# Kernel optimization log

Measured on AMD Instinct MI355X. Metric: run time of the kernel, lower is better.

Reference implementation:

```python
import jax, jax.numpy as jnp
import numpy as np

B, S, U = 64, 64, 16
EMB = 10
D = U - 2 + 2 * EMB      # encoder d_model = 34
DD = 3                   # decoder d_model
FF = 4                   # dim_feedforward
NL = 4                   # num layers (enc and dec)
ENH = 2                  # encoder heads
WV, SV = 10000, 400      # word / syllable vocab sizes


def _ln(x, w, b, eps=1e-5):
    mu = jnp.mean(x, -1, keepdims=True)
    var = jnp.mean((x - mu) ** 2, -1, keepdims=True)
    return (x - mu) / jnp.sqrt(var + eps) * w + b


def _mha(xq, xkv, qkv_w, qkv_b, out_w, out_b, nhead, mask=None):
    d = xq.shape[-1]
    wq, wk, wv = jnp.split(qkv_w, 3, axis=0)
    bq, bk, bv = jnp.split(qkv_b, 3, axis=0)
    q = xq @ wq.T + bq
    k = xkv @ wk.T + bk
    v = xkv @ wv.T + bv
    b_, sq, sk = q.shape[0], q.shape[1], k.shape[1]
    dh = d // nhead
    q = q.reshape(b_, sq, nhead, dh)
    k = k.reshape(b_, sk, nhead, dh)
    v = v.reshape(b_, sk, nhead, dh)
    scores = jnp.einsum('bqhd,bkhd->bhqk', q, k) * (1.0 / np.sqrt(dh))
    if mask is not None:
        scores = scores + mask
    attn = jax.nn.softmax(scores, axis=-1)
    out = jnp.einsum('bhqk,bkhd->bqhd', attn, v).reshape(b_, sq, d)
    return out @ out_w.T + out_b


def _pos_encoding(batch, d_model):
    # Faithful to the original quirk: pe has shape [max_len, 1, d] and is added
    # to a batch-first [B,S,D] tensor as x + pe[:B]  ->  row b of pe is added
    # to ALL sequence positions of batch element b.
    pos = jnp.arange(batch, dtype=jnp.float32)[:, None]
    div = jnp.exp(jnp.arange(0, d_model, 2, dtype=jnp.float32) * (-np.log(10000.0) / d_model))
    ang = pos * div  # [B, D/2]
    pe = jnp.stack([jnp.sin(ang), jnp.cos(ang)], axis=-1).reshape(batch, d_model)
    return pe[:, None, :]  # [B,1,D]


def setup_inputs() -> dict:
    key = jax.random.key(0)
    ks = iter(jax.random.split(key, 64))

    def n(shape, s=0.1):
        return jax.random.normal(next(ks), shape, dtype=jnp.float32) * s

    base = jax.random.uniform(next(ks), (B, S, U), dtype=jnp.float32)
    widx = jax.random.randint(next(ks), (B, S), 0, WV).astype(jnp.float32)
    sidx = jax.random.randint(next(ks), (B, S), 0, SV).astype(jnp.float32)
    src = base.at[:, :, U - 2].set(widx).at[:, :, U - 1].set(sidx)
    return {
        'src': src,
        'word_emb': jax.random.uniform(next(ks), (WV, EMB), jnp.float32, -0.1, 0.1),
        'syll_emb': jax.random.uniform(next(ks), (SV, EMB), jnp.float32, -0.1, 0.1),
        'enc_qkv_w': n((NL, 3 * D, D)), 'enc_qkv_b': jnp.zeros((NL, 3 * D)),
        'enc_out_w': n((NL, D, D)), 'enc_out_b': jnp.zeros((NL, D)),
        'enc_ln1_w': jnp.ones((NL, D)), 'enc_ln1_b': jnp.zeros((NL, D)),
        'enc_lin1_w': n((NL, FF, D)), 'enc_lin1_b': jnp.zeros((NL, FF)),
        'enc_lin2_w': n((NL, D, FF)), 'enc_lin2_b': jnp.zeros((NL, D)),
        'enc_ln2_w': jnp.ones((NL, D)), 'enc_ln2_b': jnp.zeros((NL, D)),
        'norm_w': jnp.ones((D,)), 'norm_b': jnp.zeros((D,)),
        'eo_w': jax.random.uniform(next(ks), (DD, D), jnp.float32, -0.1, 0.1),
        'eo_b': jnp.zeros((DD,)),
        'dec_sa_qkv_w': n((NL, 3 * DD, DD)), 'dec_sa_qkv_b': jnp.zeros((NL, 3 * DD)),
        'dec_sa_out_w': n((NL, DD, DD)), 'dec_sa_out_b': jnp.zeros((NL, DD)),
        'dec_ln1_w': jnp.ones((NL, DD)), 'dec_ln1_b': jnp.zeros((NL, DD)),
        'dec_ca_qkv_w': n((NL, 3 * DD, DD)), 'dec_ca_qkv_b': jnp.zeros((NL, 3 * DD)),
        'dec_ca_out_w': n((NL, DD, DD)), 'dec_ca_out_b': jnp.zeros((NL, DD)),
        'dec_ln2_w': jnp.ones((NL, DD)), 'dec_ln2_b': jnp.zeros((NL, DD)),
        'dec_lin1_w': n((NL, FF, DD)), 'dec_lin1_b': jnp.zeros((NL, FF)),
        'dec_lin2_w': n((NL, DD, FF)), 'dec_lin2_b': jnp.zeros((NL, DD)),
        'dec_ln3_w': jnp.ones((NL, DD)), 'dec_ln3_b': jnp.zeros((NL, DD)),
    }


def reference(src, word_emb, syll_emb,
              enc_qkv_w, enc_qkv_b, enc_out_w, enc_out_b,
              enc_ln1_w, enc_ln1_b, enc_lin1_w, enc_lin1_b,
              enc_lin2_w, enc_lin2_b, enc_ln2_w, enc_ln2_b,
              norm_w, norm_b, eo_w, eo_b,
              dec_sa_qkv_w, dec_sa_qkv_b, dec_sa_out_w, dec_sa_out_b,
              dec_ln1_w, dec_ln1_b,
              dec_ca_qkv_w, dec_ca_qkv_b, dec_ca_out_w, dec_ca_out_b,
              dec_ln2_w, dec_ln2_b,
              dec_lin1_w, dec_lin1_b, dec_lin2_w, dec_lin2_b,
              dec_ln3_w, dec_ln3_b):
    b, s = src.shape[0], src.shape[1]
    # embed_lyrics
    widx = src[:, :, U - 2].astype(jnp.int32)
    sidx = src[:, :, U - 1].astype(jnp.int32)
    x = jnp.concatenate([src[:, :, :U - 2], word_emb[widx], syll_emb[sidx]], axis=2)  # [B,S,D]
    x = x + _pos_encoding(b, D)
    # TransformerEncoder (post-norm, relu, dropout=0) + final LayerNorm
    for l in range(NL):
        sa = _mha(x, x, enc_qkv_w[l], enc_qkv_b[l], enc_out_w[l], enc_out_b[l], ENH)
        x = _ln(x + sa, enc_ln1_w[l], enc_ln1_b[l])
        ff = jax.nn.relu(x @ enc_lin1_w[l].T + enc_lin1_b[l]) @ enc_lin2_w[l].T + enc_lin2_b[l]
        x = _ln(x + ff, enc_ln2_w[l], enc_ln2_b[l])
    x = _ln(x, norm_w, norm_b)
    memory = x @ eo_w.T + eo_b  # [B,S,3]

    causal = jnp.where(jnp.tril(jnp.ones((s, s), bool)), 0.0, -1e9).astype(jnp.float32)

    def decode(tgt):
        y = tgt
        for l in range(NL):
            sa = _mha(y, y, dec_sa_qkv_w[l], dec_sa_qkv_b[l], dec_sa_out_w[l], dec_sa_out_b[l], 1, causal)
            y = _ln(y + sa, dec_ln1_w[l], dec_ln1_b[l])
            ca = _mha(y, memory, dec_ca_qkv_w[l], dec_ca_qkv_b[l], dec_ca_out_w[l], dec_ca_out_b[l], 1)
            y = _ln(y + ca, dec_ln2_w[l], dec_ln2_b[l])
            ff = jax.nn.relu(y @ dec_lin1_w[l].T + dec_lin1_b[l]) @ dec_lin2_w[l].T + dec_lin2_b[l]
            y = _ln(y + ff, dec_ln3_w[l], dec_ln3_b[l])
        return y

    # mask, position i only depends on tgt[:, :i+1], so a fixed-size padded
    # buffer + scan computes identical values.
    def step(tgt, i):
        out_i = jax.lax.dynamic_slice_in_dim(decode(tgt), i, 1, axis=1)  # [B,1,3]
        return jax.lax.dynamic_update_slice(tgt, out_i, (0, i + 1, 0)), None

    tgt0 = jnp.zeros((b, s, DD), jnp.float32)
    tgt, _ = jax.lax.scan(step, tgt0, jnp.arange(s - 1))
    return jnp.concatenate([tgt, src[:, :, U - 2:U - 1], src[:, :, U - 1:U]], axis=2)
```

## Files before the change

kernel.cpp:

```cpp
#include <hip/hip_runtime.h>
#include <math.h>

#define B_ 64
#define S_ 64
#define U_ 16
#define EMB_ 10
#define D_ 34
#define DD_ 3
#define FF_ 4
#define NL_ 4

__global__ __launch_bounds__(512) void enc_kernel(
    const float* __restrict__ src, const float* __restrict__ wemb,
    const float* __restrict__ semb,
    const float* __restrict__ qkv_w, const float* __restrict__ qkv_b,
    const float* __restrict__ out_w, const float* __restrict__ out_b,
    const float* __restrict__ ln1_w, const float* __restrict__ ln1_b,
    const float* __restrict__ lin1_w, const float* __restrict__ lin1_b,
    const float* __restrict__ lin2_w, const float* __restrict__ lin2_b,
    const float* __restrict__ ln2_w, const float* __restrict__ ln2_b,
    const float* __restrict__ norm_w, const float* __restrict__ norm_b,
    const float* __restrict__ eo_w, const float* __restrict__ eo_b,
    float* __restrict__ mem, float* __restrict__ out)
{
    const int b = blockIdx.x;
    const int tid = threadIdx.x;
    const int wv_ = tid >> 6;
    const int lane = tid & 63;

    __shared__ float xs[S_][D_ + 1];
    __shared__ float tmp[S_][D_ + 1];
    __shared__ float att[S_][D_ + 1];
    __shared__ __align__(16) float qsh[2][S_][21];
    __shared__ __align__(16) float ksh[2][S_][20];
    __shared__ __align__(16) float vsh[2][S_][20];
    __shared__ float ffh[S_][5];
    __shared__ float pacc[4][128][19];

    const float negln = -logf(10000.0f) / (float)D_;
    #pragma unroll
    for (int rep = 0; rep < 5; ++rep) {
        int idx = tid + rep * 512;
        if (idx < S_ * D_) {
            int pos = idx / D_, d = idx % D_;
            float v;
            if (d < U_ - 2) {
                v = src[(b * S_ + pos) * U_ + d];
            } else if (d < U_ - 2 + EMB_) {
                int wi = (int)src[(b * S_ + pos) * U_ + (U_ - 2)];
                v = wemb[wi * EMB_ + (d - (U_ - 2))];
            } else {
                int si = (int)src[(b * S_ + pos) * U_ + (U_ - 1)];
                v = semb[si * EMB_ + (d - (U_ - 2 + EMB_))];
            }
            int k = d >> 1;
            float div = __expf((float)(2 * k) * negln);
            float ang = (float)b * div;
            v += (d & 1) ? __cosf(ang) : __sinf(ang);
            xs[pos][d] = v;
        }
    }
    __syncthreads();

    const float rs17 = 0.24253562503633297f;

    for (int l = 0; l < NL_; ++l) {
        const float* Wq = qkv_w + l * 3 * D_ * D_;
        const float* Bq = qkv_b + l * 3 * D_;

        {
            float xr[D_];
            #pragma unroll
            for (int d = 0; d < D_; ++d) xr[d] = xs[lane][d];
            for (int rb = 0; rb < 13; ++rb) {
                int r = wv_ + (rb << 3);
                if (r < 3 * D_) {
                    int ru = __builtin_amdgcn_readfirstlane(r);
                    const float* wrow = Wq + ru * D_;
                    float aE = Bq[ru], aO = 0.f;
                    #pragma unroll
                    for (int d = 0; d < D_; d += 2) {
                        aE = fmaf(xr[d], wrow[d], aE);
                        aO = fmaf(xr[d + 1], wrow[d + 1], aO);
                    }
                    float acc = aE + aO;
                    if (ru < D_)          { int h = (ru >= 17), dd = ru - h * 17; qsh[h][lane][dd] = acc; }
                    else if (ru < 2 * D_) { int rr = ru - D_;     int h = (rr >= 17), dd = rr - h * 17; ksh[h][lane][dd] = acc; }
                    else                  { int rr = ru - 2 * D_; int h = (rr >= 17), dd = rr - h * 17; vsh[h][lane][dd] = acc; }
                }
            }
        }
        __syncthreads();

        {
            int c = tid >> 7, hq = tid & 127;
            int h = hq >> 6, qi = hq & 63;
            float qv[17], acc[17];
            #pragma unroll
            for (int d = 0; d < 17; ++d) { qv[d] = qsh[h][qi][d]; acc[d] = 0.f; }
            float ssum = 0.f;
            int j0 = c * 16;
            for (int jj = 0; jj < 16; ++jj) {
                int j = j0 + jj;
                const float4* kr = (const float4*)ksh[h][j];
                const float4* vr = (const float4*)vsh[h][j];
                float4 k0 = kr[0], k1 = kr[1], k2 = kr[2], k3 = kr[3];
                float  k16 = ksh[h][j][16];
                float4 v0 = vr[0], v1 = vr[1], v2 = vr[2], v3 = vr[3];
                float  v16 = vsh[h][j][16];
                float sE = qv[0]*k0.x + qv[2]*k0.z + qv[4]*k1.x + qv[6]*k1.z +
                           qv[8]*k2.x + qv[10]*k2.z + qv[12]*k3.x + qv[14]*k3.z;
                float sO = qv[1]*k0.y + qv[3]*k0.w + qv[5]*k1.y + qv[7]*k1.w +
                           qv[9]*k2.y + qv[11]*k2.w + qv[13]*k3.y + qv[15]*k3.w;
                float sc = sE + sO + qv[16]*k16;
                float e = __expf(sc * rs17);
                ssum += e;
                acc[0] += e*v0.x;  acc[1] += e*v0.y;  acc[2] += e*v0.z;  acc[3] += e*v0.w;
                acc[4] += e*v1.x;  acc[5] += e*v1.y;  acc[6] += e*v1.z;  acc[7] += e*v1.w;
                acc[8] += e*v2.x;  acc[9] += e*v2.y;  acc[10] += e*v2.z; acc[11] += e*v2.w;
                acc[12] += e*v3.x; acc[13] += e*v3.y; acc[14] += e*v3.z; acc[15] += e*v3.w;
                acc[16] += e*v16;
            }
            #pragma unroll
            for (int d = 0; d < 17; ++d) pacc[c][hq][d] = acc[d];
            pacc[c][hq][17] = ssum;
        }
        __syncthreads();

        if (tid < 128) {
            int h = tid >> 6, qi = tid & 63;
            int off = h * 17;
            float ssum = pacc[0][tid][17] + pacc[1][tid][17] +
                         pacc[2][tid][17] + pacc[3][tid][17];
            float inv = 1.f / ssum;
            #pragma unroll
            for (int d = 0; d < 17; ++d)
                att[qi][off + d] = (pacc[0][tid][d] + pacc[1][tid][d] +
                                    pacc[2][tid][d] + pacc[3][tid][d]) * inv;
        }
        __syncthreads();

        {
            float ar[D_];
            #pragma unroll
            for (int e = 0; e < D_; ++e) ar[e] = att[lane][e];
            const float* Wo = out_w + l * D_ * D_;
            const float* Bo = out_b + l * D_;
            for (int rb = 0; rb < 5; ++rb) {
                int d = wv_ + (rb << 3);
                if (d < D_) {
                    int du = __builtin_amdgcn_readfirstlane(d);
                    const float* wrow = Wo + du * D_;
                    float aE = Bo[du], aO = 0.f;
                    #pragma unroll
                    for (int e = 0; e < D_; e += 2) {
                        aE = fmaf(ar[e], wrow[e], aE);
                        aO = fmaf(ar[e + 1], wrow[e + 1], aO);
                    }
                    tmp[lane][du] = xs[lane][du] + aE + aO;
                }
            }
        }
        __syncthreads();

        if (tid < S_) {
            int row = tid;
            float sA = 0.f, sB = 0.f;
            #pragma unroll
            for (int d = 0; d < D_; d += 2) { sA += tmp[row][d]; sB += tmp[row][d + 1]; }
            float mu = (sA + sB) * (1.0f / D_);
            float vA = 0.f, vB = 0.f;
            #pragma unroll
            for (int d = 0; d < D_; d += 2) {
                float t0 = tmp[row][d] - mu;     vA += t0 * t0;
                float t1 = tmp[row][d + 1] - mu; vB += t1 * t1;
            }
            float rstd = rsqrtf((vA + vB) * (1.0f / D_) + 1e-5f);
            #pragma unroll
            for (int d = 0; d < D_; ++d)
                xs[row][d] = (tmp[row][d] - mu) * rstd * ln1_w[l * D_ + d] + ln1_b[l * D_ + d];
        }
        __syncthreads();

        if (wv_ < 4) {
            int fu = __builtin_amdgcn_readfirstlane(wv_);
            const float* wrow = lin1_w + l * FF_ * D_ + fu * D_;
            float aE = lin1_b[l * FF_ + fu], aO = 0.f;
            #pragma unroll
            for (int d = 0; d < D_; d += 2) {
                aE = fmaf(xs[lane][d], wrow[d], aE);
                aO = fmaf(xs[lane][d + 1], wrow[d + 1], aO);
            }
            ffh[lane][fu] = fmaxf(aE + aO, 0.f);
        }
        __syncthreads();

        {
            float h0 = ffh[lane][0], h1 = ffh[lane][1],
                  h2 = ffh[lane][2], h3 = ffh[lane][3];
            const float* W2 = lin2_w + l * D_ * FF_;
            const float* B2 = lin2_b + l * D_;
            for (int rb = 0; rb < 5; ++rb) {
                int d = wv_ + (rb << 3);
                if (d < D_) {
                    int du = __builtin_amdgcn_readfirstlane(d);
                    const float* wrow = W2 + du * FF_;
                    float acc = fmaf(h0, wrow[0], fmaf(h1, wrow[1],
                                fmaf(h2, wrow[2], fmaf(h3, wrow[3], B2[du]))));
                    tmp[lane][du] = xs[lane][du] + acc;
                }
            }
        }
        __syncthreads();

        if (tid < S_) {
            int row = tid;
            float sA = 0.f, sB = 0.f;
            #pragma unroll
            for (int d = 0; d < D_; d += 2) { sA += tmp[row][d]; sB += tmp[row][d + 1]; }
            float mu = (sA + sB) * (1.0f / D_);
            float vA = 0.f, vB = 0.f;
            #pragma unroll
            for (int d = 0; d < D_; d += 2) {
                float t0 = tmp[row][d] - mu;     vA += t0 * t0;
                float t1 = tmp[row][d + 1] - mu; vB += t1 * t1;
            }
            float rstd = rsqrtf((vA + vB) * (1.0f / D_) + 1e-5f);
            #pragma unroll
            for (int d = 0; d < D_; ++d)
                xs[row][d] = (tmp[row][d] - mu) * rstd * ln2_w[l * D_ + d] + ln2_b[l * D_ + d];
        }
        __syncthreads();
    }

    if (tid < S_) {
        int row = tid;
        float sA = 0.f, sB = 0.f;
        #pragma unroll
        for (int d = 0; d < D_; d += 2) { sA += xs[row][d]; sB += xs[row][d + 1]; }
        float mu = (sA + sB) * (1.0f / D_);
        float vA = 0.f, vB = 0.f;
        #pragma unroll
        for (int d = 0; d < D_; d += 2) {
            float t0 = xs[row][d] - mu;     vA += t0 * t0;
            float t1 = xs[row][d + 1] - mu; vB += t1 * t1;
        }
        float rstd = rsqrtf((vA + vB) * (1.0f / D_) + 1e-5f);
        #pragma unroll
        for (int d = 0; d < D_; ++d)
            xs[row][d] = (xs[row][d] - mu) * rstd * norm_w[d] + norm_b[d];
    }
    __syncthreads();

    if (wv_ < 3) {
        int ru = __builtin_amdgcn_readfirstlane(wv_);
        const float* wrow = eo_w + ru * D_;
        float aE = eo_b[ru], aO = 0.f;
        #pragma unroll
        for (int d = 0; d < D_; d += 2) {
            aE = fmaf(xs[lane][d], wrow[d], aE);
            aO = fmaf(xs[lane][d + 1], wrow[d + 1], aO);
        }
        mem[(b * S_ + lane) * DD_ + ru] = aE + aO;
    }

    if (tid < S_) {
        out[(b * S_ + tid) * 5 + 3] = src[(b * S_ + tid) * U_ + (U_ - 2)];
        out[(b * S_ + tid) * 5 + 4] = src[(b * S_ + tid) * U_ + (U_ - 1)];
    }
}

#define PIN(x) asm volatile("" : "+v"(x))

template <int CTRL>
__device__ __forceinline__ float dpp_add(float v) {
    int t = __builtin_amdgcn_update_dpp(0, __float_as_int(v), CTRL, 0xf, 0xf, true);
    return v + __int_as_float(t);
}

__device__ __forceinline__ float wave_sum_l63(float v) {
    v = dpp_add<0x111>(v);
    v = dpp_add<0x112>(v);
    v = dpp_add<0x114>(v);
    v = dpp_add<0x118>(v);
    v = dpp_add<0x142>(v);
    v = dpp_add<0x143>(v);
    return v;
}

__device__ __forceinline__ float bcast63(float v) {
    return __int_as_float(__builtin_amdgcn_readlane(__float_as_int(v), 63));
}

__device__ __forceinline__ void ln3e(float z0, float z1, float z2,
                                     float w0, float w1, float w2,
                                     float b0, float b1, float b2,
                                     float& o0, float& o1, float& o2) {
    float s1 = (z0 + z1) + z2;
    float s2 = fmaf(z0, z0, fmaf(z1, z1, z2 * z2));
    float mu = s1 * (1.0f / 3.0f);
    float vpe = fmaf(s2, (1.0f / 3.0f), fmaf(-mu, mu, 1e-5f));
    float rstd = __builtin_amdgcn_rsqf(vpe);
    o0 = fmaf(z0 - mu, rstd * w0, b0);
    o1 = fmaf(z1 - mu, rstd * w1, b1);
    o2 = fmaf(z2 - mu, rstd * w2, b2);
}

__global__ __launch_bounds__(64, 1) void dec_kernel(
    const float* __restrict__ mem,
    const float* __restrict__ sa_qkv_w, const float* __restrict__ sa_qkv_b,
    const float* __restrict__ sa_out_w, const float* __restrict__ sa_out_b,
    const float* __restrict__ gln1_w, const float* __restrict__ gln1_b,
    const float* __restrict__ ca_qkv_w, const float* __restrict__ ca_qkv_b,
    const float* __restrict__ ca_out_w, const float* __restrict__ ca_out_b,
    const float* __restrict__ gln2_w, const float* __restrict__ gln2_b,
    const float* __restrict__ l1_w, const float* __restrict__ l1_b,
    const float* __restrict__ l2_w, const float* __restrict__ l2_b,
    const float* __restrict__ gln3_w, const float* __restrict__ gln3_b,
    float* __restrict__ out)
{
    const int b = blockIdx.x;
    const int lane = threadIdx.x;
    const float LOG2E = 1.4426950408889634f;
    const float rs3 = 0.5773502691896258f;
    const float QS = rs3 * LOG2E;

    __shared__ __align__(16) float fst[NL_][72];
    for (int t = lane; t < NL_ * 72; t += 64) {
        int l = t / 72, s = t % 72;
        float v = 0.f;
        if      (s < 3)  v = sa_out_b[l * 3 + s];
        else if (s < 6)  v = gln1_w[l * 3 + (s - 3)];
        else if (s < 9)  v = gln1_b[l * 3 + (s - 6)];
        else if (s < 18) v = ca_qkv_w[l * 27 + (s - 9)];
        else if (s < 21) v = ca_qkv_b[l * 9 + (s - 18)];
        else if (s < 24) v = ca_out_b[l * 3 + (s - 21)];
        else if (s < 27) v = gln2_w[l * 3 + (s - 24)];
        else if (s < 30) v = gln2_b[l * 3 + (s - 27)];
        else if (s < 32) v = 0.f;
        else if (s < 44) v = l1_w[l * 12 + (s - 32)];
        else if (s < 48) v = l1_b[l * 4 + (s - 44)];
        else if (s < 60) v = l2_w[l * 12 + (s - 48)];
        else if (s < 63) v = l2_b[l * 3 + (s - 60)];
        else if (s < 66) v = gln3_w[l * 3 + (s - 63)];
        else if (s < 69) v = gln3_b[l * 3 + (s - 66)];
        fst[l][s] = v;
    }
    __syncthreads();

    float Wqp[NL_][3][3], Bqp[NL_][3];
    float Wk [NL_][3][3], Bk [NL_][3];
    float WVp[NL_][3][3], bvp[NL_][3];

    #pragma unroll
    for (int l = 0; l < NL_; ++l) {
        #pragma unroll
        for (int r = 0; r < 3; ++r) {
            Bqp[l][r] = sa_qkv_b[l * 9 + r] * QS;
            Bk [l][r] = sa_qkv_b[l * 9 + 3 + r];
            #pragma unroll
            for (int c = 0; c < 3; ++c) {
                Wqp[l][r][c] = sa_qkv_w[l * 27 + r * 3 + c] * QS;
                Wk [l][r][c] = sa_qkv_w[l * 27 + (3 + r) * 3 + c];
            }
            float a0 = 0.f, a1 = 0.f, a2 = 0.f, ab = 0.f;
            #pragma unroll
            for (int t = 0; t < 3; ++t) {
                float wso = sa_out_w[l * 9 + r * 3 + t];
                a0 += wso * sa_qkv_w[l * 27 + (6 + t) * 3 + 0];
                a1 += wso * sa_qkv_w[l * 27 + (6 + t) * 3 + 1];
                a2 += wso * sa_qkv_w[l * 27 + (6 + t) * 3 + 2];
                ab += wso * sa_qkv_b[l * 9 + 6 + t];
            }
            WVp[l][r][0] = a0; WVp[l][r][1] = a1; WVp[l][r][2] = a2;
            bvp[l][r] = ab;
        }
    }

    float m0 = mem[(b * S_ + lane) * DD_ + 0];
    float m1 = mem[(b * S_ + lane) * DD_ + 1];
    float m2 = mem[(b * S_ + lane) * DD_ + 2];

    float ck[NL_][3], cvp[NL_][3];
    #pragma unroll
    for (int l = 0; l < NL_; ++l) {
        float cvt[3];
        #pragma unroll
        for (int t = 0; t < 3; ++t) {
            cvt[t] = ca_qkv_w[l * 27 + (6 + t) * 3 + 0] * m0 +
                     ca_qkv_w[l * 27 + (6 + t) * 3 + 1] * m1 +
                     ca_qkv_w[l * 27 + (6 + t) * 3 + 2] * m2 + ca_qkv_b[l * 9 + 6 + t];
        }
        #pragma unroll
        for (int r = 0; r < 3; ++r) {
            float kk = ca_qkv_w[l * 27 + (3 + r) * 3 + 0] * m0 +
                       ca_qkv_w[l * 27 + (3 + r) * 3 + 1] * m1 +
                       ca_qkv_w[l * 27 + (3 + r) * 3 + 2] * m2 + ca_qkv_b[l * 9 + 3 + r];
            ck[l][r] = kk * QS;
            cvp[l][r] = ca_out_w[l * 9 + r * 3 + 0] * cvt[0] +
                        ca_out_w[l * 9 + r * 3 + 1] * cvt[1] +
                        ca_out_w[l * 9 + r * 3 + 2] * cvt[2];
        }
    }

    #pragma unroll
    for (int l = 0; l < NL_; ++l) {
        #pragma unroll
        for (int r = 0; r < 3; ++r) {
            PIN(Bqp[l][r]); PIN(Bk[l][r]); PIN(bvp[l][r]);
            PIN(ck[l][r]); PIN(cvp[l][r]);
            #pragma unroll
            for (int c = 0; c < 3; ++c) {
                PIN(Wqp[l][r][c]); PIN(Wk[l][r][c]); PIN(WVp[l][r][c]);
            }
        }
    }

    float sk[NL_][3] = {{0.f}}, sv[NL_][3] = {{0.f}};

    if (lane < 3) out[(b * S_ + 0) * 5 + lane] = 0.f;

    float y0 = 0.f, y1 = 0.f, y2 = 0.f;

    for (int i = 0; i < S_ - 1; ++i) {
        float msa = (lane <= i) ? 0.f : -1.0e30f;
        #pragma unroll
        for (int l = 0; l < NL_; ++l) {
            float wa[32];
            {
                const float4* fp = (const float4*)fst[l];
                #pragma unroll
                for (int k = 0; k < 8; ++k) {
                    float4 t4 = fp[k];
                    wa[4 * k + 0] = t4.x; wa[4 * k + 1] = t4.y;
                    wa[4 * k + 2] = t4.z; wa[4 * k + 3] = t4.w;
                }
            }

            float q0 = fmaf(Wqp[l][0][0], y0, fmaf(Wqp[l][0][1], y1, fmaf(Wqp[l][0][2], y2, Bqp[l][0])));
            float q1 = fmaf(Wqp[l][1][0], y0, fmaf(Wqp[l][1][1], y1, fmaf(Wqp[l][1][2], y2, Bqp[l][1])));
            float q2 = fmaf(Wqp[l][2][0], y0, fmaf(Wqp[l][2][1], y1, fmaf(Wqp[l][2][2], y2, Bqp[l][2])));
            float k0 = fmaf(Wk[l][0][0], y0, fmaf(Wk[l][0][1], y1, fmaf(Wk[l][0][2], y2, Bk[l][0])));
            float k1 = fmaf(Wk[l][1][0], y0, fmaf(Wk[l][1][1], y1, fmaf(Wk[l][1][2], y2, Bk[l][1])));
            float k2 = fmaf(Wk[l][2][0], y0, fmaf(Wk[l][2][1], y1, fmaf(Wk[l][2][2], y2, Bk[l][2])));
            float v0 = fmaf(WVp[l][0][0], y0, fmaf(WVp[l][0][1], y1, fmaf(WVp[l][0][2], y2, bvp[l][0])));
            float v1 = fmaf(WVp[l][1][0], y0, fmaf(WVp[l][1][1], y1, fmaf(WVp[l][1][2], y2, bvp[l][1])));
            float v2 = fmaf(WVp[l][2][0], y0, fmaf(WVp[l][2][1], y1, fmaf(WVp[l][2][2], y2, bvp[l][2])));
            if (lane == i) {
                sk[l][0] = k0; sk[l][1] = k1; sk[l][2] = k2;
                sv[l][0] = v0; sv[l][1] = v1; sv[l][2] = v2;
            }
            float sc = fmaf(q0, sk[l][0], fmaf(q1, sk[l][1], fmaf(q2, sk[l][2], msa)));
            float e = __builtin_amdgcn_exp2f(sc);

            float wb[40];
            {
                const float4* fp = (const float4*)&fst[l][32];
                #pragma unroll
                for (int k = 0; k < 10; ++k) {
                    float4 t4 = fp[k];
                    wb[4 * k + 0] = t4.x; wb[4 * k + 1] = t4.y;
                    wb[4 * k + 2] = t4.z; wb[4 * k + 3] = t4.w;
                }
            }

            float es  = bcast63(wave_sum_l63(e));
            float ev0 = bcast63(wave_sum_l63(e * sv[l][0]));
            float ev1 = bcast63(wave_sum_l63(e * sv[l][1]));
            float ev2 = bcast63(wave_sum_l63(e * sv[l][2]));
            float t0 = y0 + wa[0], t1 = y1 + wa[1], t2 = y2 + wa[2];
            float z0 = fmaf(t0, es, ev0);
            float z1 = fmaf(t1, es, ev1);
            float z2 = fmaf(t2, es, ev2);
            ln3e(z0, z1, z2, wa[3], wa[4], wa[5], wa[6], wa[7], wa[8],
                 y0, y1, y2);

            float p0 = fmaf(wa[9],  y0, fmaf(wa[10], y1, fmaf(wa[11], y2, wa[18])));
            float p1 = fmaf(wa[12], y0, fmaf(wa[13], y1, fmaf(wa[14], y2, wa[19])));
            float p2 = fmaf(wa[15], y0, fmaf(wa[16], y1, fmaf(wa[17], y2, wa[20])));
            float sc2 = fmaf(p0, ck[l][0], fmaf(p1, ck[l][1], p2 * ck[l][2]));
            float e2 = __builtin_amdgcn_exp2f(sc2);
            float cs  = bcast63(wave_sum_l63(e2));
            float cw0 = bcast63(wave_sum_l63(e2 * cvp[l][0]));
            float cw1 = bcast63(wave_sum_l63(e2 * cvp[l][1]));
            float cw2 = bcast63(wave_sum_l63(e2 * cvp[l][2]));
            float u0 = y0 + wa[21], u1 = y1 + wa[22], u2 = y2 + wa[23];
            z0 = fmaf(u0, cs, cw0);
            z1 = fmaf(u1, cs, cw1);
            z2 = fmaf(u2, cs, cw2);
            ln3e(z0, z1, z2, wa[24], wa[25], wa[26], wa[27], wa[28], wa[29],
                 y0, y1, y2);

            float h0 = fmaxf(fmaf(wb[0], y0, fmaf(wb[1],  y1, fmaf(wb[2],  y2, wb[12]))), 0.f);
            float h1 = fmaxf(fmaf(wb[3], y0, fmaf(wb[4],  y1, fmaf(wb[5],  y2, wb[13]))), 0.f);
            float h2 = fmaxf(fmaf(wb[6], y0, fmaf(wb[7],  y1, fmaf(wb[8],  y2, wb[14]))), 0.f);
            float h3 = fmaxf(fmaf(wb[9], y0, fmaf(wb[10], y1, fmaf(wb[11], y2, wb[15]))), 0.f);
            float f0 = fmaf(wb[16], h0, fmaf(wb[17], h1, fmaf(wb[18], h2, fmaf(wb[19], h3, wb[28]))));
            float f1 = fmaf(wb[20], h0, fmaf(wb[21], h1, fmaf(wb[22], h2, fmaf(wb[23], h3, wb[29]))));
            float f2 = fmaf(wb[24], h0, fmaf(wb[25], h1, fmaf(wb[26], h2, fmaf(wb[27], h3, wb[30]))));
            ln3e(y0 + f0, y1 + f1, y2 + f2, wb[31], wb[32], wb[33],
                 wb[34], wb[35], wb[36], y0, y1, y2);
        }
        if (lane == 0) {
            out[(b * S_ + i + 1) * 5 + 0] = y0;
            out[(b * S_ + i + 1) * 5 + 1] = y1;
            out[(b * S_ + i + 1) * 5 + 2] = y2;
        }
    }
}

extern "C" void kernel_launch(void* const* d_in, const int* in_sizes, int n_in,
                              void* d_out, int out_size, void* d_ws, size_t ws_size,
                              hipStream_t stream) {
    const float* src  = (const float*)d_in[0];
    const float* wemb = (const float*)d_in[1];
    const float* semb = (const float*)d_in[2];

    float* mem = (float*)d_ws;
    float* out = (float*)d_out;

    enc_kernel<<<B_, 512, 0, stream>>>(
        src, wemb, semb,
        (const float*)d_in[3],  (const float*)d_in[4],
        (const float*)d_in[5],  (const float*)d_in[6],
        (const float*)d_in[7],  (const float*)d_in[8],
        (const float*)d_in[9],  (const float*)d_in[10],
        (const float*)d_in[11], (const float*)d_in[12],
        (const float*)d_in[13], (const float*)d_in[14],
        (const float*)d_in[15], (const float*)d_in[16],
        (const float*)d_in[17], (const float*)d_in[18],
        mem, out);

    dec_kernel<<<B_, 64, 0, stream>>>(
        mem,
        (const float*)d_in[19], (const float*)d_in[20],
        (const float*)d_in[21], (const float*)d_in[22],
        (const float*)d_in[23], (const float*)d_in[24],
        (const float*)d_in[25], (const float*)d_in[26],
        (const float*)d_in[27], (const float*)d_in[28],
        (const float*)d_in[29], (const float*)d_in[30],
        (const float*)d_in[31], (const float*)d_in[32],
        (const float*)d_in[33], (const float*)d_in[34],
        (const float*)d_in[35], (const float*)d_in[36],
        out);
}
```

Measured before the change: 366.5 us.

## Undo folded attention algebra in decoder; hold more weights in registers

The decoder stops folding the self-attention value projection into the output projection, and stops folding the normalisation and out-projection into the LayerNorm. It now computes the softmax-weighted average explicitly, using a reciprocal of the sum, and then applies the out projection. Most per-layer weights move from shared memory into pinned registers, so the shared-memory table keeps only the FFN and LN3 parameters. This adds reciprocal and extra 3x3 matvec work per step and raises register pressure, in exchange for fewer LDS loads per step.

```diff
diff --git a/kernel.cpp b/kernel.cpp
--- a/kernel.cpp
+++ b/kernel.cpp
@@ -325,55 +325,49 @@
     const float rs3 = 0.5773502691896258f;
     const float QS = rs3 * LOG2E;
 
-    __shared__ __align__(16) float fst[NL_][72];
-    for (int t = lane; t < NL_ * 72; t += 64) {
-        int l = t / 72, s = t % 72;
+    __shared__ __align__(16) float fst[NL_][40];
+    for (int t = lane; t < NL_ * 40; t += 64) {
+        int l = t / 40, s = t % 40;
         float v = 0.f;
-        if      (s < 3)  v = sa_out_b[l * 3 + s];
-        else if (s < 6)  v = gln1_w[l * 3 + (s - 3)];
-        else if (s < 9)  v = gln1_b[l * 3 + (s - 6)];
-        else if (s < 18) v = ca_qkv_w[l * 27 + (s - 9)];
-        else if (s < 21) v = ca_qkv_b[l * 9 + (s - 18)];
-        else if (s < 24) v = ca_out_b[l * 3 + (s - 21)];
-        else if (s < 27) v = gln2_w[l * 3 + (s - 24)];
-        else if (s < 30) v = gln2_b[l * 3 + (s - 27)];
-        else if (s < 32) v = 0.f;
-        else if (s < 44) v = l1_w[l * 12 + (s - 32)];
-        else if (s < 48) v = l1_b[l * 4 + (s - 44)];
-        else if (s < 60) v = l2_w[l * 12 + (s - 48)];
-        else if (s < 63) v = l2_b[l * 3 + (s - 60)];
-        else if (s < 66) v = gln3_w[l * 3 + (s - 63)];
-        else if (s < 69) v = gln3_b[l * 3 + (s - 66)];
+        if      (s < 12) v = l1_w[l * 12 + s];
+        else if (s < 16) v = l1_b[l * 4 + (s - 12)];
+        else if (s < 28) v = l2_w[l * 12 + (s - 16)];
+        else if (s < 31) v = l2_b[l * 3 + (s - 28)];
+        else if (s < 34) v = gln3_w[l * 3 + (s - 31)];
+        else if (s < 37) v = gln3_b[l * 3 + (s - 34)];
         fst[l][s] = v;
     }
     __syncthreads();
 
-    float Wqp[NL_][3][3], Bqp[NL_][3];
-    float Wk [NL_][3][3], Bk [NL_][3];
-    float WVp[NL_][3][3], bvp[NL_][3];
+    float Wsq[NL_][9][3], Bsq[NL_][9];
+    float Wso[NL_][3][3], Bso[NL_][3];
+    float N1w[NL_][3], N1b[NL_][3];
+    float Wcq[NL_][3][3], Bcq[NL_][3];
+    float Wco[NL_][3][3], Bco[NL_][3];
+    float N2w[NL_][3], N2b[NL_][3];
 
     #pragma unroll
     for (int l = 0; l < NL_; ++l) {
         #pragma unroll
+        for (int r = 0; r < 9; ++r) {
+            float sc = (r < 3) ? QS : 1.0f;
+            Bsq[l][r] = sa_qkv_b[l * 9 + r] * sc;
+            #pragma unroll
+            for (int c = 0; c < 3; ++c) Wsq[l][r][c] = sa_qkv_w[l * 27 + r * 3 + c] * sc;
+        }
+        #pragma unroll
         for (int r = 0; r < 3; ++r) {
-            Bqp[l][r] = sa_qkv_b[l * 9 + r] * QS;
-            Bk [l][r] = sa_qkv_b[l * 9 + 3 + r];
+            Bso[l][r] = sa_out_b[l * 3 + r];
+            Bcq[l][r] = ca_qkv_b[l * 9 + r] * QS;
+            Bco[l][r] = ca_out_b[l * 3 + r];
+            N1w[l][r] = gln1_w[l * 3 + r];  N1b[l][r] = gln1_b[l * 3 + r];
+            N2w[l][r] = gln2_w[l * 3 + r];  N2b[l][r] = gln2_b[l * 3 + r];
             #pragma unroll
             for (int c = 0; c < 3; ++c) {
-                Wqp[l][r][c] = sa_qkv_w[l * 27 + r * 3 + c] * QS;
-                Wk [l][r][c] = sa_qkv_w[l * 27 + (3 + r) * 3 + c];
-            }
-            float a0 = 0.f, a1 = 0.f, a2 = 0.f, ab = 0.f;
-            #pragma unroll
-            for (int t = 0; t < 3; ++t) {
-                float wso = sa_out_w[l * 9 + r * 3 + t];
-                a0 += wso * sa_qkv_w[l * 27 + (6 + t) * 3 + 0];
-                a1 += wso * sa_qkv_w[l * 27 + (6 + t) * 3 + 1];
-                a2 += wso * sa_qkv_w[l * 27 + (6 + t) * 3 + 2];
-                ab += wso * sa_qkv_b[l * 9 + 6 + t];
-            }
-            WVp[l][r][0] = a0; WVp[l][r][1] = a1; WVp[l][r][2] = a2;
-            bvp[l][r] = ab;
+                Wso[l][r][c] = sa_out_w[l * 9 + r * 3 + c];
+                Wcq[l][r][c] = ca_qkv_w[l * 27 + r * 3 + c] * QS;
+                Wco[l][r][c] = ca_out_w[l * 9 + r * 3 + c];
+            }
         }
     }
 
@@ -381,38 +375,34 @@
     float m1 = mem[(b * S_ + lane) * DD_ + 1];
     float m2 = mem[(b * S_ + lane) * DD_ + 2];
 
-    float ck[NL_][3], cvp[NL_][3];
+    float ck[NL_][3], cv[NL_][3];
     #pragma unroll
     for (int l = 0; l < NL_; ++l) {
-        float cvt[3];
-        #pragma unroll
-        for (int t = 0; t < 3; ++t) {
-            cvt[t] = ca_qkv_w[l * 27 + (6 + t) * 3 + 0] * m0 +
-                     ca_qkv_w[l * 27 + (6 + t) * 3 + 1] * m1 +
-                     ca_qkv_w[l * 27 + (6 + t) * 3 + 2] * m2 + ca_qkv_b[l * 9 + 6 + t];
-        }
         #pragma unroll
         for (int r = 0; r < 3; ++r) {
-            float kk = ca_qkv_w[l * 27 + (3 + r) * 3 + 0] * m0 +
+            ck[l][r] = ca_qkv_w[l * 27 + (3 + r) * 3 + 0] * m0 +
                        ca_qkv_w[l * 27 + (3 + r) * 3 + 1] * m1 +
                        ca_qkv_w[l * 27 + (3 + r) * 3 + 2] * m2 + ca_qkv_b[l * 9 + 3 + r];
-            ck[l][r] = kk * QS;
-            cvp[l][r] = ca_out_w[l * 9 + r * 3 + 0] * cvt[0] +
-                        ca_out_w[l * 9 + r * 3 + 1] * cvt[1] +
-                        ca_out_w[l * 9 + r * 3 + 2] * cvt[2];
+            cv[l][r] = ca_qkv_w[l * 27 + (6 + r) * 3 + 0] * m0 +
+                       ca_qkv_w[l * 27 + (6 + r) * 3 + 1] * m1 +
+                       ca_qkv_w[l * 27 + (6 + r) * 3 + 2] * m2 + ca_qkv_b[l * 9 + 6 + r];
         }
     }
 
     #pragma unroll
     for (int l = 0; l < NL_; ++l) {
         #pragma unroll
+        for (int r = 0; r < 9; ++r) {
+            PIN(Bsq[l][r]);
+            #pragma unroll
+            for (int c = 0; c < 3; ++c) PIN(Wsq[l][r][c]);
+        }
+        #pragma unroll
         for (int r = 0; r < 3; ++r) {
-            PIN(Bqp[l][r]); PIN(Bk[l][r]); PIN(bvp[l][r]);
-            PIN(ck[l][r]); PIN(cvp[l][r]);
-            #pragma unroll
-            for (int c = 0; c < 3; ++c) {
-                PIN(Wqp[l][r][c]); PIN(Wk[l][r][c]); PIN(WVp[l][r][c]);
-            }
+            PIN(Bso[l][r]); PIN(Bcq[l][r]); PIN(Bco[l][r]);
+            PIN(N1w[l][r]); PIN(N1b[l][r]); PIN(N2w[l][r]); PIN(N2b[l][r]);
+            #pragma unroll
+            for (int c = 0; c < 3; ++c) { PIN(Wso[l][r][c]); PIN(Wcq[l][r][c]); PIN(Wco[l][r][c]); }
         }
     }
 
@@ -426,80 +416,73 @@
         float msa = (lane <= i) ? 0.f : -1.0e30f;
         #pragma unroll
         for (int l = 0; l < NL_; ++l) {
-            float wa[32];
+            float wv[40];
             {
                 const float4* fp = (const float4*)fst[l];
                 #pragma unroll
-                for (int k = 0; k < 8; ++k) {
-                    float4 t4 = fp[k];
-                    wa[4 * k + 0] = t4.x; wa[4 * k + 1] = t4.y;
-                    wa[4 * k + 2] = t4.z; wa[4 * k + 3] = t4.w;
-                }
-            }
-
-            float q0 = fmaf(Wqp[l][0][0], y0, fmaf(Wqp[l][0][1], y1, fmaf(Wqp[l][0][2], y2, Bqp[l][0])));
-            float q1 = fmaf(Wqp[l][1][0], y0, fmaf(Wqp[l][1][1], y1, fmaf(Wqp[l][1][2], y2, Bqp[l][1])));
-            float q2 = fmaf(Wqp[l][2][0], y0, fmaf(Wqp[l][2][1], y1, fmaf(Wqp[l][2][2], y2, Bqp[l][2])));
-            float k0 = fmaf(Wk[l][0][0], y0, fmaf(Wk[l][0][1], y1, fmaf(Wk[l][0][2], y2, Bk[l][0])));
-            float k1 = fmaf(Wk[l][1][0], y0, fmaf(Wk[l][1][1], y1, fmaf(Wk[l][1][2], y2, Bk[l][1])));
-            float k2 = fmaf(Wk[l][2][0], y0, fmaf(Wk[l][2][1], y1, fmaf(Wk[l][2][2], y2, Bk[l][2])));
-            float v0 = fmaf(WVp[l][0][0], y0, fmaf(WVp[l][0][1], y1, fmaf(WVp[l][0][2], y2, bvp[l][0])));
-            float v1 = fmaf(WVp[l][1][0], y0, fmaf(WVp[l][1][1], y1, fmaf(WVp[l][1][2], y2, bvp[l][1])));
-            float v2 = fmaf(WVp[l][2][0], y0, fmaf(WVp[l][2][1], y1, fmaf(WVp[l][2][2], y2, bvp[l][2])));
-            if (lane == i) {
-                sk[l][0] = k0; sk[l][1] = k1; sk[l][2] = k2;
-                sv[l][0] = v0; sv[l][1] = v1; sv[l][2] = v2;
-            }
-            float sc = fmaf(q0, sk[l][0], fmaf(q1, sk[l][1], fmaf(q2, sk[l][2], msa)));
-            float e = __builtin_amdgcn_exp2f(sc);
-
-            float wb[40];
-            {
-                const float4* fp = (const float4*)&fst[l][32];
-                #pragma unroll
                 for (int k = 0; k < 10; ++k) {
                     float4 t4 = fp[k];
-                    wb[4 * k + 0] = t4.x; wb[4 * k + 1] = t4.y;
-                    wb[4 * k + 2] = t4.z; wb[4 * k + 3] = t4.w;
+                    wv[4 * k + 0] = t4.x; wv[4 * k + 1] = t4.y;
+                    wv[4 * k + 2] = t4.z; wv[4 * k + 3] = t4.w;
                 }
-            }
-
-            float es  = bcast63(wave_sum_l63(e));
-            float ev0 = bcast63(wave_sum_l63(e * sv[l][0]));
-            float ev1 = bcast63(wave_sum_l63(e * sv[l][1]));
-            float ev2 = bcast63(wave_sum_l63(e * sv[l][2]));
-            float t0 = y0 + wa[0], t1 = y1 + wa[1], t2 = y2 + wa[2];
-            float z0 = fmaf(t0, es, ev0);
-            float z1 = fmaf(t1, es, ev1);
-            float z2 = fmaf(t2, es, ev2);
-            ln3e(z0, z1, z2, wa[3], wa[4], wa[5], wa[6], wa[7], wa[8],
+                #pragma unroll
+                for (int k = 0; k < 37; ++k) PIN(wv[k]);
+            }
+
+            float q[3], kn[3], vn[3];
+            #pragma unroll
+            for (int r = 0; r < 3; ++r) {
+                q[r]  = fmaf(Wsq[l][r][0], y0, fmaf(Wsq[l][r][1], y1, fmaf(Wsq[l][r][2], y2, Bsq[l][r])));
+                kn[r] = fmaf(Wsq[l][3 + r][0], y0, fmaf(Wsq[l][3 + r][1], y1, fmaf(Wsq[l][3 + r][2], y2, Bsq[l][3 + r])));
+                vn[r] = fmaf(Wsq[l][6 + r][0], y0, fmaf(Wsq[l][6 + r][1], y1, fmaf(Wsq[l][6 + r][2], y2, Bsq[l][6 + r])));
+            }
+            if (lane == i) {
+                #pragma unroll
+                for (int r = 0; r < 3; ++r) { sk[l][r] = kn[r]; sv[l][r] = vn[r]; }
+            }
+            float sc = fmaf(q[0], sk[l][0], fmaf(q[1], sk[l][1], fmaf(q[2], sk[l][2], msa)));
+            float e = __builtin_amdgcn_exp2f(sc);
+            float es  = wave_sum_l63(e);
+            float ev0 = wave_sum_l63(e * sv[l][0]);
+            float ev1 = wave_sum_l63(e * sv[l][1]);
+            float ev2 = wave_sum_l63(e * sv[l][2]);
+            float inv = __builtin_amdgcn_rcpf(bcast63(es));
+            float a0 = bcast63(ev0) * inv, a1 = bcast63(ev1) * inv, a2 = bcast63(ev2) * inv;
+            float s0 = fmaf(Wso[l][0][0], a0, fmaf(Wso[l][0][1], a1, fmaf(Wso[l][0][2], a2, Bso[l][0])));
+            float s1 = fmaf(Wso[l][1][0], a0, fmaf(Wso[l][1][1], a1, fmaf(Wso[l][1][2], a2, Bso[l][1])));
+            float s2 = fmaf(Wso[l][2][0], a0, fmaf(Wso[l][2][1], a1, fmaf(Wso[l][2][2], a2, Bso[l][2])));
+            ln3e(y0 + s0, y1 + s1, y2 + s2,
+                 N1w[l][0], N1w[l][1], N1w[l][2], N1b[l][0], N1b[l][1], N1b[l][2],
                  y0, y1, y2);
 
-            float p0 = fmaf(wa[9],  y0, fmaf(wa[10], y1, fmaf(wa[11], y2, wa[18])));
-            float p1 = fmaf(wa[12], y0, fmaf(wa[13], y1, fmaf(wa[14], y2, wa[19])));
-            float p2 = fmaf(wa[15], y0, fmaf(wa[16], y1, fmaf(wa[17], y2, wa[20])));
+            float p0 = fmaf(Wcq[l][0][0], y0, fmaf(Wcq[l][0][1], y1, fmaf(Wcq[l][0][2], y2, Bcq[l][0])));
+            float p1 = fmaf(Wcq[l][1][0], y0, fmaf(Wcq[l][1][1], y1, fmaf(Wcq[l][1][2], y2, Bcq[l][1])));
+            float p2 = fmaf(Wcq[l][2][0], y0, fmaf(Wcq[l][2][1], y1, fmaf(Wcq[l][2][2], y2, Bcq[l][2])));
             float sc2 = fmaf(p0, ck[l][0], fmaf(p1, ck[l][1], p2 * ck[l][2]));
             float e2 = __builtin_amdgcn_exp2f(sc2);
-            float cs  = bcast63(wave_sum_l63(e2));
-            float cw0 = bcast63(wave_sum_l63(e2 * cvp[l][0]));
-            float cw1 = bcast63(wave_sum_l63(e2 * cvp[l][1]));
-            float cw2 = bcast63(wave_sum_l63(e2 * cvp[l][2]));
-            float u0 = y0 + wa[21], u1 = y1 + wa[22], u2 = y2 + wa[23];
-            z0 = fmaf(u0, cs, cw0);
-            z1 = fmaf(u1, cs, cw1);
-            z2 = fmaf(u2, cs, cw2);
-            ln3e(z0, z1, z2, wa[24], wa[25], wa[26], wa[27], wa[28], wa[29],
+            float cs  = wave_sum_l63(e2);
+            float cw0 = wave_sum_l63(e2 * cv[l][0]);
+            float cw1 = wave_sum_l63(e2 * cv[l][1]);
+            float cw2 = wave_sum_l63(e2 * cv[l][2]);
+            inv = __builtin_amdgcn_rcpf(bcast63(cs));
+            a0 = bcast63(cw0) * inv; a1 = bcast63(cw1) * inv; a2 = bcast63(cw2) * inv;
+            float c0 = fmaf(Wco[l][0][0], a0, fmaf(Wco[l][0][1], a1, fmaf(Wco[l][0][2], a2, Bco[l][0])));
+            float c1 = fmaf(Wco[l][1][0], a0, fmaf(Wco[l][1][1], a1, fmaf(Wco[l][1][2], a2, Bco[l][1])));
+            float c2 = fmaf(Wco[l][2][0], a0, fmaf(Wco[l][2][1], a1, fmaf(Wco[l][2][2], a2, Bco[l][2])));
+            ln3e(y0 + c0, y1 + c1, y2 + c2,
+                 N2w[l][0], N2w[l][1], N2w[l][2], N2b[l][0], N2b[l][1], N2b[l][2],
                  y0, y1, y2);
 
-            float h0 = fmaxf(fmaf(wb[0], y0, fmaf(wb[1],  y1, fmaf(wb[2],  y2, wb[12]))), 0.f);
-            float h1 = fmaxf(fmaf(wb[3], y0, fmaf(wb[4],  y1, fmaf(wb[5],  y2, wb[13]))), 0.f);
-            float h2 = fmaxf(fmaf(wb[6], y0, fmaf(wb[7],  y1, fmaf(wb[8],  y2, wb[14]))), 0.f);
-            float h3 = fmaxf(fmaf(wb[9], y0, fmaf(wb[10], y1, fmaf(wb[11], y2, wb[15]))), 0.f);
-            float f0 = fmaf(wb[16], h0, fmaf(wb[17], h1, fmaf(wb[18], h2, fmaf(wb[19], h3, wb[28]))));
-            float f1 = fmaf(wb[20], h0, fmaf(wb[21], h1, fmaf(wb[22], h2, fmaf(wb[23], h3, wb[29]))));
-            float f2 = fmaf(wb[24], h0, fmaf(wb[25], h1, fmaf(wb[26], h2, fmaf(wb[27], h3, wb[30]))));
-            ln3e(y0 + f0, y1 + f1, y2 + f2, wb[31], wb[32], wb[33],
-                 wb[34], wb[35], wb[36], y0, y1, y2);
+            float h0 = fmaxf(fmaf(wv[0], y0, fmaf(wv[1],  y1, fmaf(wv[2],  y2, wv[12]))), 0.f);
+            float h1 = fmaxf(fmaf(wv[3], y0, fmaf(wv[4],  y1, fmaf(wv[5],  y2, wv[13]))), 0.f);
+            float h2 = fmaxf(fmaf(wv[6], y0, fmaf(wv[7],  y1, fmaf(wv[8],  y2, wv[14]))), 0.f);
+            float h3 = fmaxf(fmaf(wv[9], y0, fmaf(wv[10], y1, fmaf(wv[11], y2, wv[15]))), 0.f);
+            float f0 = fmaf(wv[16], h0, fmaf(wv[17], h1, fmaf(wv[18], h2, fmaf(wv[19], h3, wv[28]))));
+            float f1 = fmaf(wv[20], h0, fmaf(wv[21], h1, fmaf(wv[22], h2, fmaf(wv[23], h3, wv[29]))));
+            float f2 = fmaf(wv[24], h0, fmaf(wv[25], h1, fmaf(wv[26], h2, fmaf(wv[27], h3, wv[30]))));
+            ln3e(y0 + f0, y1 + f1, y2 + f2,
+                 wv[31], wv[32], wv[33], wv[34], wv[35], wv[36],
+                 y0, y1, y2);
         }
         if (lane == 0) {
             out[(b * S_ + i + 1) * 5 + 0] = y0;
```

Result: faster. 348.6 us (-4.9%).
